# Kernel tuning notes

Hardware: AMD Instinct MI355X
Metric: run time of the kernel (lower is better)

## Reference

```python
import jax, jax.numpy as jnp
import numpy as np

EPS = 1e-5
CONV_THRESHOLD = 0.0


def setup_inputs() -> dict:
    key = jax.random.key(0)
    ks = jax.random.split(key, 16)
    B, F = 65536, 256
    H1, H2 = 1024, 512
    d_in = F + 1  # raw features + 1 scalar conv feature
    inp = {
        "x": jax.random.normal(ks[0], (B, F), dtype=jnp.float32),
        # layer 1: Linear(d_in, H1) + BatchNorm1d(H1)
        "W1": jax.random.normal(ks[1], (d_in, H1), dtype=jnp.float32) * (1.0 / np.sqrt(d_in)),
        "b1": jax.random.normal(ks[2], (H1,), dtype=jnp.float32) * 0.01,
        "g1": jnp.ones((H1,), jnp.float32) + 0.1 * jax.random.normal(ks[3], (H1,), dtype=jnp.float32),
        "be1": jax.random.normal(ks[4], (H1,), dtype=jnp.float32) * 0.01,
        "m1": jax.random.normal(ks[5], (H1,), dtype=jnp.float32) * 0.1,
        "v1": jax.random.uniform(ks[6], (H1,), dtype=jnp.float32, minval=0.5, maxval=1.5),
        # layer 2: Linear(H1, H2) + BatchNorm1d(H2)
        "W2": jax.random.normal(ks[7], (H1, H2), dtype=jnp.float32) * (1.0 / np.sqrt(H1)),
        "b2": jax.random.normal(ks[8], (H2,), dtype=jnp.float32) * 0.01,
        "g2": jnp.ones((H2,), jnp.float32) + 0.1 * jax.random.normal(ks[9], (H2,), dtype=jnp.float32),
        "be2": jax.random.normal(ks[10], (H2,), dtype=jnp.float32) * 0.01,
        "m2": jax.random.normal(ks[11], (H2,), dtype=jnp.float32) * 0.1,
        "v2": jax.random.uniform(ks[12], (H2,), dtype=jnp.float32, minval=0.5, maxval=1.5),
        # output head: Linear(H2, 1)
        "W3": jax.random.normal(ks[13], (H2, 1), dtype=jnp.float32) * (1.0 / np.sqrt(H2)),
        "b3": jax.random.normal(ks[14], (1,), dtype=jnp.float32) * 0.01,
    }
    return inp


def _bn(h, g, be, m, v):
    # eval-mode BatchNorm1d with running statistics
    return g * (h - m) * jax.lax.rsqrt(v + EPS) + be


def reference(x, W1, b1, g1, be1, m1, v1, W2, b2, g2, be2, m2, v2, W3, b3):
    # Batched replacement of the per-sample numpy threshold conv:
    # the Conv filter reduces the whole sample patch with a mean and thresholds it,
    # producing one binary scalar feature per sample.  [B, 1]
    conv_feat = jnp.where(jnp.mean(x, axis=1, keepdims=True) > CONV_THRESHOLD, 1.0, 0.0).astype(x.dtype)
    h = jnp.concatenate([x, conv_feat], axis=1)  # [B, F+1]
    h = jax.nn.relu(_bn(h @ W1 + b1, g1, be1, m1, v1))  # [B, H1]
    h = jax.nn.relu(_bn(h @ W2 + b2, g2, be2, m2, v2))  # [B, H2]
    return jax.nn.sigmoid(h @ W3 + b3)  # [B, 1]
```

## Files before the change

kernel.cpp:

```cpp
#include <hip/hip_runtime.h>
#include <hip/hip_bf16.h>
#include <hip/hip_cooperative_groups.h>
#include <cstdint>
#include <cstddef>

namespace cg = cooperative_groups;

typedef __bf16 bf16_t;
typedef bf16_t bf16x8 __attribute__((ext_vector_type(8)));
typedef float f32x4 __attribute__((ext_vector_type(4)));

#define BN_EPS 1e-5f

__device__ __forceinline__ void async_load16(const bf16_t* g, bf16_t* lds) {
  __builtin_amdgcn_global_load_lds(
      (__attribute__((address_space(1))) uint32_t*)(g),
      (__attribute__((address_space(3))) uint32_t*)(lds),
      16, 0, 0);
}

__global__ void prep_weights_kernel(const float* __restrict__ W1, const float* __restrict__ W2,
                                    const float* b1, const float* g1, const float* be1,
                                    const float* m1, const float* v1,
                                    const float* b2, const float* g2, const float* be2,
                                    const float* m2, const float* v2,
                                    bf16_t* __restrict__ W1T, bf16_t* __restrict__ W2T,
                                    float* s1, float* t1, float* s2, float* t2,
                                    float* w1last) {
  const int b = blockIdx.x;
  if (b < 192) {
    const float* src;
    bf16_t* dst;
    int R, C, bx, by;
    if (b < 64) { src = W1; dst = W1T; R = 256; C = 1024; bx = b & 15; by = b >> 4; }
    else        { src = W2; dst = W2T; R = 1024; C = 512; bx = (b - 64) & 7; by = (b - 64) >> 3; }
    __shared__ bf16_t tile[64][66];
    const int r0 = by * 64, c0 = bx * 64;
    const int tc = threadIdx.x & 63;
    const int tr4 = threadIdx.x >> 6;
#pragma unroll
    for (int i = 0; i < 16; ++i) {
      int r = i * 4 + tr4;
      tile[r][tc] = (bf16_t)src[(size_t)(r0 + r) * C + c0 + tc];
    }
    __syncthreads();
#pragma unroll
    for (int i = 0; i < 16; ++i) {
      int rr = i * 4 + tr4;
      dst[(size_t)(c0 + rr) * R + r0 + tc] = tile[tc][rr];
    }
  } else {
    for (int i = threadIdx.x; i < 1024; i += 256) {
      float s = g1[i] * rsqrtf(v1[i] + BN_EPS);
      s1[i] = s;
      t1[i] = be1[i] - m1[i] * s + b1[i] * s;
      w1last[i] = W1[256 * 1024 + i];
      if (i < 512) {
        float s2v = g2[i] * rsqrtf(v2[i] + BN_EPS);
        s2[i] = s2v;
        t2[i] = be2[i] - m2[i] * s2v + b2[i] * s2v;
      }
    }
  }
}

__device__ __forceinline__ void gemm1_body(
    const float* __restrict__ x, const bf16_t* __restrict__ W1T,
    const float* __restrict__ s1, const float* __restrict__ t1,
    const float* __restrict__ w1last, bf16_t* __restrict__ h1,
    unsigned char* smem, int mTile, int lane, int w) {
  bf16_t* As = (bf16_t*)smem;
  bf16_t* Bs = (bf16_t*)(smem + 65536);
  float* convs = (float*)(smem + 65536);
  const int l15 = lane & 15;
  const int quad = lane >> 4;

  {
    const int rsub = lane >> 5;
    const int c = lane & 31;
#pragma unroll
    for (int i = 0; i < 16; ++i) {
      int row = w * 32 + i * 2 + rsub;
      const float* gx = x + (size_t)(mTile + row) * 256 + c * 8;
      const float4 a = *(const float4*)gx;
      const float4 bq = *(const float4*)(gx + 4);
      float s = a.x + a.y + a.z + a.w + bq.x + bq.y + bq.z + bq.w;
      bf16x8 v = {(bf16_t)a.x, (bf16_t)a.y, (bf16_t)a.z, (bf16_t)a.w,
                  (bf16_t)bq.x, (bf16_t)bq.y, (bf16_t)bq.z, (bf16_t)bq.w};
      *(bf16x8*)(As + row * 256 + (c ^ (row & 7)) * 8) = v;
#pragma unroll
      for (int m = 1; m <= 16; m <<= 1) s += __shfl_xor(s, m);
      if (c == 0) convs[row] = (s > 0.0f) ? 1.0f : 0.0f;
    }
  }
  __syncthreads();

  unsigned cmask = 0;
#pragma unroll
  for (int ti = 0; ti < 8; ++ti)
#pragma unroll
    for (int r = 0; r < 4; ++r)
      if (convs[ti * 16 + quad * 4 + r] > 0.5f) cmask |= (1u << (ti * 4 + r));
  __syncthreads();

  bf16_t* BsW = Bs + w * 2048;
  const int srow = lane >> 2;
  const int schunk = (lane & 3) ^ ((lane >> 3) & 3);
  const int rchunk = quad ^ ((l15 >> 1) & 3);

  for (int j = 0; j < 4; ++j) {
    const int colbase = j * 256 + w * 64;
    f32x4 acc[8][4];
#pragma unroll
    for (int i = 0; i < 8; ++i)
#pragma unroll
      for (int t = 0; t < 4; ++t) {
        f32x4 z = {0.f, 0.f, 0.f, 0.f};
        acc[i][t] = z;
      }

    const bf16_t* gB = W1T + (size_t)(colbase + srow) * 256 + schunk * 8;

#pragma unroll
    for (int i = 0; i < 4; ++i)
      async_load16(gB + (size_t)(i * 16) * 256, BsW + i * 512 + lane * 8);

    for (int ks = 0; ks < 8; ++ks) {
      asm volatile("s_waitcnt vmcnt(0)" ::: "memory");

      bf16x8 af[8], bfr[4];
#pragma unroll
      for (int tj = 0; tj < 4; ++tj)
        bfr[tj] = *(const bf16x8*)(BsW + (tj * 16 + l15) * 32 + rchunk * 8);
#pragma unroll
      for (int ti = 0; ti < 8; ++ti)
        af[ti] = *(const bf16x8*)(As + (ti * 16 + l15) * 256 + ((ks * 4 + quad) ^ (l15 & 7)) * 8);

      asm volatile("s_waitcnt lgkmcnt(0)" ::: "memory");
      if (ks < 7) {
#pragma unroll
        for (int i = 0; i < 4; ++i)
          async_load16(gB + (size_t)(i * 16) * 256 + (ks + 1) * 32, BsW + i * 512 + lane * 8);
      }

      __builtin_amdgcn_s_setprio(1);
#pragma unroll
      for (int ti = 0; ti < 8; ++ti)
#pragma unroll
        for (int tj = 0; tj < 4; ++tj)
          acc[ti][tj] = __builtin_amdgcn_mfma_f32_16x16x32_bf16(af[ti], bfr[tj], acc[ti][tj], 0, 0, 0);
      __builtin_amdgcn_s_setprio(0);
    }

    float sc[4], tcv[4], wl[4];
#pragma unroll
    for (int tj = 0; tj < 4; ++tj) {
      int c = colbase + tj * 16 + l15;
      sc[tj] = s1[c];
      tcv[tj] = t1[c];
      wl[tj] = w1last[c];
    }
#pragma unroll
    for (int ti = 0; ti < 8; ++ti)
#pragma unroll
      for (int r = 0; r < 4; ++r) {
        int row = mTile + ti * 16 + quad * 4 + r;
        size_t base = (size_t)row * 1024 + colbase;
        const float cfv = ((cmask >> (ti * 4 + r)) & 1u) ? 1.0f : 0.0f;
#pragma unroll
        for (int tj = 0; tj < 4; ++tj) {
          float z = acc[ti][tj][r] + cfv * wl[tj];
          z = fmaxf(z * sc[tj] + tcv[tj], 0.f);
          h1[base + tj * 16 + l15] = (bf16_t)z;
        }
      }
  }
}

__device__ __forceinline__ void gemm2_task_body(
    const bf16_t* __restrict__ h1, const bf16_t* __restrict__ W2T,
    const float* __restrict__ s2, const float* __restrict__ t2,
    const float* __restrict__ W3, float* __restrict__ partials,
    unsigned char* smem, int task, int lane, int w) {
  bf16_t* As2 = (bf16_t*)smem;
  bf16_t* Bs2 = (bf16_t*)(smem + 49152);
  const int l15 = lane & 15;
  const int quad = lane >> 4;
  const int sRow = lane >> 2;
  const int sColSwz = ((lane & 3) ^ ((lane >> 3) & 3)) * 8;
  const int rchunk8 = (quad ^ ((l15 >> 1) & 3)) * 8;

  const int mt = (task >> 5) * 8 + (task & 7);
  const int mTile2 = mt * 256;
  const int nt = (task >> 3) & 3;
  const int nTile = nt * 128;

  const bf16_t* gA = h1 + (size_t)(mTile2 + w * 64 + sRow) * 1024 + sColSwz;
  const bf16_t* gB = W2T + (size_t)(nTile + w * 32 + sRow) * 1024 + sColSwz;
  bf16_t* lA0 = As2 + (w * 64) * 32;
  bf16_t* lB0 = Bs2 + (w * 32) * 32;

  f32x4 acc[4][8];
#pragma unroll
  for (int i = 0; i < 4; ++i)
#pragma unroll
    for (int j = 0; j < 8; ++j) {
      f32x4 z = {0.f, 0.f, 0.f, 0.f};
      acc[i][j] = z;
    }

  __syncthreads();

#define STAGE2(aoff, boff, k0)                                              \
  do {                                                                      \
    bf16_t* lA = lA0 + (aoff);                                              \
    bf16_t* lB = lB0 + (boff);                                              \
    async_load16(gA + (k0), lA);                                            \
    async_load16(gA + (size_t)16 * 1024 + (k0), lA + 16 * 32);              \
    async_load16(gA + (size_t)32 * 1024 + (k0), lA + 32 * 32);              \
    async_load16(gA + (size_t)48 * 1024 + (k0), lA + 48 * 32);              \
    async_load16(gB + (k0), lB);                                            \
    async_load16(gB + (size_t)16 * 1024 + (k0), lB + 16 * 32);              \
  } while (0)

  STAGE2(0, 0, 0);
  STAGE2(8192, 4096, 32);

  int aCur = 0, aN1 = 8192, aN2 = 16384;
  int bCur = 0, bN1 = 4096, bN2 = 8192;

  for (int t = 0; t < 32; ++t) {
    if (t < 30) {
      STAGE2(aN2, bN2, (t + 2) * 32);
      asm volatile("s_waitcnt vmcnt(12)" ::: "memory");
    } else if (t == 30) {
      asm volatile("s_waitcnt vmcnt(6)" ::: "memory");
    } else {
      asm volatile("s_waitcnt vmcnt(0)" ::: "memory");
    }
    asm volatile("s_barrier" ::: "memory");

    bf16x8 af[4], bfr[8];
#pragma unroll
    for (int ti = 0; ti < 4; ++ti)
      af[ti] = *(const bf16x8*)(As2 + aCur + (w * 64 + ti * 16 + l15) * 32 + rchunk8);
#pragma unroll
    for (int tj = 0; tj < 8; ++tj)
      bfr[tj] = *(const bf16x8*)(Bs2 + bCur + (tj * 16 + l15) * 32 + rchunk8);

    __builtin_amdgcn_s_setprio(1);
#pragma unroll
    for (int ti = 0; ti < 4; ++ti)
#pragma unroll
      for (int tj = 0; tj < 8; ++tj)
        acc[ti][tj] = __builtin_amdgcn_mfma_f32_16x16x32_bf16(af[ti], bfr[tj], acc[ti][tj], 0, 0, 0);
    __builtin_amdgcn_s_setprio(0);

    asm volatile("s_barrier" ::: "memory");

    int tmp = aCur; aCur = aN1; aN1 = aN2; aN2 = tmp;
    tmp = bCur; bCur = bN1; bN1 = bN2; bN2 = tmp;
  }
#undef STAGE2

  float sc[8], tcs[8], w3c[8];
#pragma unroll
  for (int tj = 0; tj < 8; ++tj) {
    int c = nTile + tj * 16 + l15;
    sc[tj] = s2[c];
    tcs[tj] = t2[c];
    w3c[tj] = W3[c];
  }
#pragma unroll
  for (int ti = 0; ti < 4; ++ti)
#pragma unroll
    for (int r = 0; r < 4; ++r) {
      float pv = 0.f;
#pragma unroll
      for (int tj = 0; tj < 8; ++tj) {
        float z = fmaxf(acc[ti][tj][r] * sc[tj] + tcs[tj], 0.f);
        pv += z * w3c[tj];
      }
#pragma unroll
      for (int m = 1; m <= 8; m <<= 1) pv += __shfl_xor(pv, m);
      if (l15 == 0)
        partials[(size_t)nt * 65536 + mTile2 + w * 64 + ti * 16 + quad * 4 + r] = pv;
    }
}

__global__ __launch_bounds__(256, 2) void gemm1_kernel(
    const float* __restrict__ x, const bf16_t* __restrict__ W1T,
    const float* __restrict__ s1, const float* __restrict__ t1,
    const float* __restrict__ w1last, bf16_t* __restrict__ h1) {
  __shared__ __align__(16) unsigned char smem[81920];
  gemm1_body(x, W1T, s1, t1, w1last, h1, smem, blockIdx.x * 128,
             threadIdx.x & 63, threadIdx.x >> 6);
}

__global__ __launch_bounds__(256, 2) void gemm2_kernel(
    const bf16_t* __restrict__ h1, const bf16_t* __restrict__ W2T,
    const float* __restrict__ s2, const float* __restrict__ t2,
    const float* __restrict__ W3, float* __restrict__ partials) {
  __shared__ __align__(16) unsigned char smem[73728];
  gemm2_task_body(h1, W2T, s2, t2, W3, partials, smem, blockIdx.x,
                  threadIdx.x & 63, threadIdx.x >> 6);
}

__global__ void sigmoid_partials_kernel(const float* __restrict__ partials,
                                        const float* __restrict__ b3,
                                        float* __restrict__ out) {
  int i = blockIdx.x * 256 + threadIdx.x;
  float z = partials[i] + partials[65536 + i] + partials[2 * 65536 + i] +
            partials[3 * 65536 + i] + b3[0];
  out[i] = 1.0f / (1.0f + expf(-z));
}

__global__ __launch_bounds__(256, 2) void fused_mlp_coop(
    const float* __restrict__ x,
    const bf16_t* __restrict__ W1T, const bf16_t* __restrict__ W2T,
    const float* __restrict__ s1, const float* __restrict__ t1,
    const float* __restrict__ w1last,
    const float* __restrict__ s2, const float* __restrict__ t2,
    const float* __restrict__ W3, const float* __restrict__ b3,
    bf16_t* __restrict__ h1, float* __restrict__ partials,
    float* __restrict__ out) {
  __shared__ __align__(16) unsigned char smem[81920];
  cg::grid_group grid = cg::this_grid();
  const int tid = threadIdx.x;
  const int lane = tid & 63;
  const int w = tid >> 6;

  gemm1_body(x, W1T, s1, t1, w1last, h1, smem, blockIdx.x * 128, lane, w);

  grid.sync();

  gemm2_task_body(h1, W2T, s2, t2, W3, partials, smem, blockIdx.x, lane, w);
  gemm2_task_body(h1, W2T, s2, t2, W3, partials, smem, blockIdx.x + 512, lane, w);

  grid.sync();

  if (tid < 128) {
    int r = blockIdx.x * 128 + tid;
    float z = partials[r] + partials[65536 + r] + partials[2 * 65536 + r] +
              partials[3 * 65536 + r] + b3[0];
    out[r] = 1.0f / (1.0f + expf(-z));
  }
}

extern "C" void kernel_launch(void* const* d_in, const int* in_sizes, int n_in,
                              void* d_out, int out_size, void* d_ws, size_t ws_size,
                              hipStream_t stream) {
  const float* x = (const float*)d_in[0];
  const float* W1 = (const float*)d_in[1];
  const float* b1 = (const float*)d_in[2];
  const float* g1 = (const float*)d_in[3];
  const float* be1 = (const float*)d_in[4];
  const float* m1 = (const float*)d_in[5];
  const float* v1 = (const float*)d_in[6];
  const float* W2 = (const float*)d_in[7];
  const float* b2 = (const float*)d_in[8];
  const float* g2 = (const float*)d_in[9];
  const float* be2 = (const float*)d_in[10];
  const float* m2 = (const float*)d_in[11];
  const float* v2 = (const float*)d_in[12];
  const float* W3 = (const float*)d_in[13];
  const float* b3 = (const float*)d_in[14];
  float* out = (float*)d_out;

  char* p = (char*)d_ws;
  bf16_t* h1 = (bf16_t*)p;       p += (size_t)65536 * 1024 * 2;
  float* partials = (float*)p;   p += (size_t)4 * 65536 * 4;
  bf16_t* W1T = (bf16_t*)p;      p += (size_t)1024 * 256 * 2;
  bf16_t* W2T = (bf16_t*)p;      p += (size_t)512 * 1024 * 2;
  float* w1last = (float*)p;     p += 1024 * 4;
  float* s1 = (float*)p;         p += 1024 * 4;
  float* t1 = (float*)p;         p += 1024 * 4;
  float* s2 = (float*)p;         p += 512 * 4;
  float* t2 = (float*)p;         p += 512 * 4;

  prep_weights_kernel<<<193, 256, 0, stream>>>(W1, W2, b1, g1, be1, m1, v1,
                                               b2, g2, be2, m2, v2,
                                               W1T, W2T, s1, t1, s2, t2, w1last);

  int dev = 0;
  (void)hipGetDevice(&dev);
  int coopOk = 0;
  (void)hipDeviceGetAttribute(&coopOk, hipDeviceAttributeCooperativeLaunch, dev);
  int numCU = 0;
  (void)hipDeviceGetAttribute(&numCU, hipDeviceAttributeMultiprocessorCount, dev);
  int maxBlk = 0;
  (void)hipOccupancyMaxActiveBlocksPerMultiprocessor(&maxBlk, fused_mlp_coop, 256, 0);

  bool useCoop = (coopOk != 0) && ((long)maxBlk * (long)numCU >= 512L);
  if (useCoop) {
    void* args[] = {(void*)&x, (void*)&W1T, (void*)&W2T, (void*)&s1, (void*)&t1,
                    (void*)&w1last, (void*)&s2, (void*)&t2, (void*)&W3, (void*)&b3,
                    (void*)&h1, (void*)&partials, (void*)&out};
    hipError_t e = hipLaunchCooperativeKernel((const void*)fused_mlp_coop,
                                              dim3(512), dim3(256), args, 0, stream);
    if (e != hipSuccess) useCoop = false;
  }
  if (!useCoop) {
    gemm1_kernel<<<512, 256, 0, stream>>>(x, W1T, s1, t1, w1last, h1);
    gemm2_kernel<<<1024, 256, 0, stream>>>(h1, W2T, s2, t2, W3, partials);
    sigmoid_partials_kernel<<<256, 256, 0, stream>>>(partials, b3, out);
  }
}
```

Measured before the change: 262.6 us.

## Fuse both GEMMs per 64-row tile, drop cooperative grid syncs

Replaces the cooperative kernel and its two grid-wide syncs with a normal 1024-block kernel. Each block computes its own 64-row slice of h1, then immediately runs the second GEMM on those rows, which are likely still in L2. The output head and sigmoid run in-block, so the global partials buffer goes away. Smaller tiles allow three blocks per CU, but each block now reloads all of W2T and the second GEMM uses a 64x256 tile with double buffering, which lowers reuse of the weights.

Measured after the change: 261.5 us. Within noise of the previous version (-0.4%).

```diff
diff --git a/kernel.cpp b/kernel.cpp
--- a/kernel.cpp
+++ b/kernel.cpp
@@ -1,10 +1,7 @@
 #include <hip/hip_runtime.h>
 #include <hip/hip_bf16.h>
-#include <hip/hip_cooperative_groups.h>
 #include <cstdint>
 #include <cstddef>
-
-namespace cg = cooperative_groups;
 
 typedef __bf16 bf16_t;
 typedef bf16_t bf16x8 __attribute__((ext_vector_type(8)));
@@ -64,23 +61,32 @@
   }
 }
 
-__device__ __forceinline__ void gemm1_body(
-    const float* __restrict__ x, const bf16_t* __restrict__ W1T,
+__global__ __launch_bounds__(256, 3) void fused_mlp(
+    const float* __restrict__ x,
+    const bf16_t* __restrict__ W1T, const bf16_t* __restrict__ W2T,
     const float* __restrict__ s1, const float* __restrict__ t1,
-    const float* __restrict__ w1last, bf16_t* __restrict__ h1,
-    unsigned char* smem, int mTile, int lane, int w) {
-  bf16_t* As = (bf16_t*)smem;
-  bf16_t* Bs = (bf16_t*)(smem + 65536);
-  float* convs = (float*)(smem + 65536);
+    const float* __restrict__ w1last,
+    const float* __restrict__ s2, const float* __restrict__ t2,
+    const float* __restrict__ W3, const float* __restrict__ b3,
+    bf16_t* __restrict__ h1, float* __restrict__ out) {
+  __shared__ __align__(16) unsigned char smem[49152];
+  const int tid = threadIdx.x;
+  const int lane = tid & 63;
+  const int w = tid >> 6;
   const int l15 = lane & 15;
   const int quad = lane >> 4;
+  const int mTile = blockIdx.x * 64;
+
+  bf16_t* As = (bf16_t*)smem;
+  bf16_t* Bs = (bf16_t*)(smem + 32768);
+  float* convs = (float*)(smem + 32768);
 
   {
     const int rsub = lane >> 5;
     const int c = lane & 31;
 #pragma unroll
-    for (int i = 0; i < 16; ++i) {
-      int row = w * 32 + i * 2 + rsub;
+    for (int i = 0; i < 8; ++i) {
+      int row = w * 16 + i * 2 + rsub;
       const float* gx = x + (size_t)(mTile + row) * 256 + c * 8;
       const float4 a = *(const float4*)gx;
       const float4 bq = *(const float4*)(gx + 4);
@@ -97,7 +103,7 @@
 
   unsigned cmask = 0;
 #pragma unroll
-  for (int ti = 0; ti < 8; ++ti)
+  for (int ti = 0; ti < 4; ++ti)
 #pragma unroll
     for (int r = 0; r < 4; ++r)
       if (convs[ti * 16 + quad * 4 + r] > 0.5f) cmask |= (1u << (ti * 4 + r));
@@ -110,9 +116,9 @@
 
   for (int j = 0; j < 4; ++j) {
     const int colbase = j * 256 + w * 64;
-    f32x4 acc[8][4];
-#pragma unroll
-    for (int i = 0; i < 8; ++i)
+    f32x4 acc[4][4];
+#pragma unroll
+    for (int i = 0; i < 4; ++i)
 #pragma unroll
       for (int t = 0; t < 4; ++t) {
         f32x4 z = {0.f, 0.f, 0.f, 0.f};
@@ -128,12 +134,12 @@
     for (int ks = 0; ks < 8; ++ks) {
       asm volatile("s_waitcnt vmcnt(0)" ::: "memory");
 
-      bf16x8 af[8], bfr[4];
+      bf16x8 af[4], bfr[4];
 #pragma unroll
       for (int tj = 0; tj < 4; ++tj)
         bfr[tj] = *(const bf16x8*)(BsW + (tj * 16 + l15) * 32 + rchunk * 8);
 #pragma unroll
-      for (int ti = 0; ti < 8; ++ti)
+      for (int ti = 0; ti < 4; ++ti)
         af[ti] = *(const bf16x8*)(As + (ti * 16 + l15) * 256 + ((ks * 4 + quad) ^ (l15 & 7)) * 8);
 
       asm volatile("s_waitcnt lgkmcnt(0)" ::: "memory");
@@ -145,7 +151,7 @@
 
       __builtin_amdgcn_s_setprio(1);
 #pragma unroll
-      for (int ti = 0; ti < 8; ++ti)
+      for (int ti = 0; ti < 4; ++ti)
 #pragma unroll
         for (int tj = 0; tj < 4; ++tj)
           acc[ti][tj] = __builtin_amdgcn_mfma_f32_16x16x32_bf16(af[ti], bfr[tj], acc[ti][tj], 0, 0, 0);
@@ -161,7 +167,7 @@
       wl[tj] = w1last[c];
     }
 #pragma unroll
-    for (int ti = 0; ti < 8; ++ti)
+    for (int ti = 0; ti < 4; ++ti)
 #pragma unroll
       for (int r = 0; r < 4; ++r) {
         int row = mTile + ti * 16 + quad * 4 + r;
@@ -175,175 +181,115 @@
         }
       }
   }
-}
-
-__device__ __forceinline__ void gemm2_task_body(
-    const bf16_t* __restrict__ h1, const bf16_t* __restrict__ W2T,
-    const float* __restrict__ s2, const float* __restrict__ t2,
-    const float* __restrict__ W3, float* __restrict__ partials,
-    unsigned char* smem, int task, int lane, int w) {
-  bf16_t* As2 = (bf16_t*)smem;
-  bf16_t* Bs2 = (bf16_t*)(smem + 49152);
-  const int l15 = lane & 15;
-  const int quad = lane >> 4;
-  const int sRow = lane >> 2;
-  const int sColSwz = ((lane & 3) ^ ((lane >> 3) & 3)) * 8;
-  const int rchunk8 = (quad ^ ((l15 >> 1) & 3)) * 8;
-
-  const int mt = (task >> 5) * 8 + (task & 7);
-  const int mTile2 = mt * 256;
-  const int nt = (task >> 3) & 3;
-  const int nTile = nt * 128;
-
-  const bf16_t* gA = h1 + (size_t)(mTile2 + w * 64 + sRow) * 1024 + sColSwz;
-  const bf16_t* gB = W2T + (size_t)(nTile + w * 32 + sRow) * 1024 + sColSwz;
-  bf16_t* lA0 = As2 + (w * 64) * 32;
-  bf16_t* lB0 = Bs2 + (w * 32) * 32;
-
-  f32x4 acc[4][8];
-#pragma unroll
-  for (int i = 0; i < 4; ++i)
-#pragma unroll
-    for (int j = 0; j < 8; ++j) {
-      f32x4 z = {0.f, 0.f, 0.f, 0.f};
-      acc[i][j] = z;
-    }
-
+
+  asm volatile("s_waitcnt vmcnt(0)" ::: "memory");
+
+  bf16_t* A2 = (bf16_t*)smem;
+  bf16_t* B2 = (bf16_t*)(smem + 8192);
+  float* outW = (float*)(smem + 40960);
+  const int rchunk8 = rchunk * 8;
+  const int sColSwz = schunk * 8;
+
+  float rowpv[4][4];
+#pragma unroll
+  for (int ti = 0; ti < 4; ++ti)
+#pragma unroll
+    for (int r = 0; r < 4; ++r) rowpv[ti][r] = 0.f;
+
+  for (int nt = 0; nt < 2; ++nt) {
+    __syncthreads();
+
+    const bf16_t* gA = h1 + (size_t)(mTile + w * 16 + srow) * 1024 + sColSwz;
+    const bf16_t* gB2 = W2T + (size_t)(nt * 256 + w * 64 + srow) * 1024 + sColSwz;
+
+    f32x4 acc2[4][4];
+#pragma unroll
+    for (int i = 0; i < 4; ++i)
+#pragma unroll
+      for (int t = 0; t < 4; ++t) {
+        f32x4 z = {0.f, 0.f, 0.f, 0.f};
+        acc2[i][t] = z;
+      }
+
+#define STAGE2(buf, k0)                                                       \
+  do {                                                                        \
+    async_load16(gA + (k0), A2 + (buf)*2048 + w * 512 + lane * 8);            \
+    async_load16(gB2 + (k0), B2 + (buf)*8192 + w * 2048 + lane * 8);          \
+    async_load16(gB2 + (size_t)16 * 1024 + (k0),                              \
+                 B2 + (buf)*8192 + w * 2048 + 512 + lane * 8);                \
+    async_load16(gB2 + (size_t)32 * 1024 + (k0),                              \
+                 B2 + (buf)*8192 + w * 2048 + 1024 + lane * 8);               \
+    async_load16(gB2 + (size_t)48 * 1024 + (k0),                              \
+                 B2 + (buf)*8192 + w * 2048 + 1536 + lane * 8);               \
+  } while (0)
+
+    STAGE2(0, 0);
+    int buf = 0;
+    for (int t = 0; t < 32; ++t) {
+      if (t < 31) {
+        STAGE2(buf ^ 1, (t + 1) * 32);
+        asm volatile("s_waitcnt vmcnt(5)" ::: "memory");
+      } else {
+        asm volatile("s_waitcnt vmcnt(0)" ::: "memory");
+      }
+      asm volatile("s_barrier" ::: "memory");
+
+      bf16x8 af[4], bfr[4];
+#pragma unroll
+      for (int ti = 0; ti < 4; ++ti)
+        af[ti] = *(const bf16x8*)(A2 + buf * 2048 + (ti * 16 + l15) * 32 + rchunk8);
+#pragma unroll
+      for (int tj = 0; tj < 4; ++tj)
+        bfr[tj] = *(const bf16x8*)(B2 + buf * 8192 + (w * 64 + tj * 16 + l15) * 32 + rchunk8);
+
+      __builtin_amdgcn_s_setprio(1);
+#pragma unroll
+      for (int ti = 0; ti < 4; ++ti)
+#pragma unroll
+        for (int tj = 0; tj < 4; ++tj)
+          acc2[ti][tj] = __builtin_amdgcn_mfma_f32_16x16x32_bf16(af[ti], bfr[tj], acc2[ti][tj], 0, 0, 0);
+      __builtin_amdgcn_s_setprio(0);
+
+      asm volatile("s_barrier" ::: "memory");
+      buf ^= 1;
+    }
+#undef STAGE2
+
+    float sc[4], tcs[4], w3c[4];
+#pragma unroll
+    for (int tj = 0; tj < 4; ++tj) {
+      int c = nt * 256 + w * 64 + tj * 16 + l15;
+      sc[tj] = s2[c];
+      tcs[tj] = t2[c];
+      w3c[tj] = W3[c];
+    }
+#pragma unroll
+    for (int ti = 0; ti < 4; ++ti)
+#pragma unroll
+      for (int r = 0; r < 4; ++r) {
+        float pv = 0.f;
+#pragma unroll
+        for (int tj = 0; tj < 4; ++tj) {
+          float z = fmaxf(acc2[ti][tj][r] * sc[tj] + tcs[tj], 0.f);
+          pv += z * w3c[tj];
+        }
+#pragma unroll
+        for (int m = 1; m <= 8; m <<= 1) pv += __shfl_xor(pv, m);
+        rowpv[ti][r] += pv;
+      }
+  }
+
+  if (l15 == 0) {
+#pragma unroll
+    for (int ti = 0; ti < 4; ++ti)
+#pragma unroll
+      for (int r = 0; r < 4; ++r)
+        outW[w * 64 + ti * 16 + quad * 4 + r] = rowpv[ti][r];
+  }
   __syncthreads();
-
-#define STAGE2(aoff, boff, k0)                                              \
-  do {                                                                      \
-    bf16_t* lA = lA0 + (aoff);                                              \
-    bf16_t* lB = lB0 + (boff);                                              \
-    async_load16(gA + (k0), lA);                                            \
-    async_load16(gA + (size_t)16 * 1024 + (k0), lA + 16 * 32);              \
-    async_load16(gA + (size_t)32 * 1024 + (k0), lA + 32 * 32);              \
-    async_load16(gA + (size_t)48 * 1024 + (k0), lA + 48 * 32);              \
-    async_load16(gB + (k0), lB);                                            \
-    async_load16(gB + (size_t)16 * 1024 + (k0), lB + 16 * 32);              \
-  } while (0)
-
-  STAGE2(0, 0, 0);
-  STAGE2(8192, 4096, 32);
-
-  int aCur = 0, aN1 = 8192, aN2 = 16384;
-  int bCur = 0, bN1 = 4096, bN2 = 8192;
-
-  for (int t = 0; t < 32; ++t) {
-    if (t < 30) {
-      STAGE2(aN2, bN2, (t + 2) * 32);
-      asm volatile("s_waitcnt vmcnt(12)" ::: "memory");
-    } else if (t == 30) {
-      asm volatile("s_waitcnt vmcnt(6)" ::: "memory");
-    } else {
-      asm volatile("s_waitcnt vmcnt(0)" ::: "memory");
-    }
-    asm volatile("s_barrier" ::: "memory");
-
-    bf16x8 af[4], bfr[8];
-#pragma unroll
-    for (int ti = 0; ti < 4; ++ti)
-      af[ti] = *(const bf16x8*)(As2 + aCur + (w * 64 + ti * 16 + l15) * 32 + rchunk8);
-#pragma unroll
-    for (int tj = 0; tj < 8; ++tj)
-      bfr[tj] = *(const bf16x8*)(Bs2 + bCur + (tj * 16 + l15) * 32 + rchunk8);
-
-    __builtin_amdgcn_s_setprio(1);
-#pragma unroll
-    for (int ti = 0; ti < 4; ++ti)
-#pragma unroll
-      for (int tj = 0; tj < 8; ++tj)
-        acc[ti][tj] = __builtin_amdgcn_mfma_f32_16x16x32_bf16(af[ti], bfr[tj], acc[ti][tj], 0, 0, 0);
-    __builtin_amdgcn_s_setprio(0);
-
-    asm volatile("s_barrier" ::: "memory");
-
-    int tmp = aCur; aCur = aN1; aN1 = aN2; aN2 = tmp;
-    tmp = bCur; bCur = bN1; bN1 = bN2; bN2 = tmp;
-  }
-#undef STAGE2
-
-  float sc[8], tcs[8], w3c[8];
-#pragma unroll
-  for (int tj = 0; tj < 8; ++tj) {
-    int c = nTile + tj * 16 + l15;
-    sc[tj] = s2[c];
-    tcs[tj] = t2[c];
-    w3c[tj] = W3[c];
-  }
-#pragma unroll
-  for (int ti = 0; ti < 4; ++ti)
-#pragma unroll
-    for (int r = 0; r < 4; ++r) {
-      float pv = 0.f;
-#pragma unroll
-      for (int tj = 0; tj < 8; ++tj) {
-        float z = fmaxf(acc[ti][tj][r] * sc[tj] + tcs[tj], 0.f);
-        pv += z * w3c[tj];
-      }
-#pragma unroll
-      for (int m = 1; m <= 8; m <<= 1) pv += __shfl_xor(pv, m);
-      if (l15 == 0)
-        partials[(size_t)nt * 65536 + mTile2 + w * 64 + ti * 16 + quad * 4 + r] = pv;
-    }
-}
-
-__global__ __launch_bounds__(256, 2) void gemm1_kernel(
-    const float* __restrict__ x, const bf16_t* __restrict__ W1T,
-    const float* __restrict__ s1, const float* __restrict__ t1,
-    const float* __restrict__ w1last, bf16_t* __restrict__ h1) {
-  __shared__ __align__(16) unsigned char smem[81920];
-  gemm1_body(x, W1T, s1, t1, w1last, h1, smem, blockIdx.x * 128,
-             threadIdx.x & 63, threadIdx.x >> 6);
-}
-
-__global__ __launch_bounds__(256, 2) void gemm2_kernel(
-    const bf16_t* __restrict__ h1, const bf16_t* __restrict__ W2T,
-    const float* __restrict__ s2, const float* __restrict__ t2,
-    const float* __restrict__ W3, float* __restrict__ partials) {
-  __shared__ __align__(16) unsigned char smem[73728];
-  gemm2_task_body(h1, W2T, s2, t2, W3, partials, smem, blockIdx.x,
-                  threadIdx.x & 63, threadIdx.x >> 6);
-}
-
-__global__ void sigmoid_partials_kernel(const float* __restrict__ partials,
-                                        const float* __restrict__ b3,
-                                        float* __restrict__ out) {
-  int i = blockIdx.x * 256 + threadIdx.x;
-  float z = partials[i] + partials[65536 + i] + partials[2 * 65536 + i] +
-            partials[3 * 65536 + i] + b3[0];
-  out[i] = 1.0f / (1.0f + expf(-z));
-}
-
-__global__ __launch_bounds__(256, 2) void fused_mlp_coop(
-    const float* __restrict__ x,
-    const bf16_t* __restrict__ W1T, const bf16_t* __restrict__ W2T,
-    const float* __restrict__ s1, const float* __restrict__ t1,
-    const float* __restrict__ w1last,
-    const float* __restrict__ s2, const float* __restrict__ t2,
-    const float* __restrict__ W3, const float* __restrict__ b3,
-    bf16_t* __restrict__ h1, float* __restrict__ partials,
-    float* __restrict__ out) {
-  __shared__ __align__(16) unsigned char smem[81920];
-  cg::grid_group grid = cg::this_grid();
-  const int tid = threadIdx.x;
-  const int lane = tid & 63;
-  const int w = tid >> 6;
-
-  gemm1_body(x, W1T, s1, t1, w1last, h1, smem, blockIdx.x * 128, lane, w);
-
-  grid.sync();
-
-  gemm2_task_body(h1, W2T, s2, t2, W3, partials, smem, blockIdx.x, lane, w);
-  gemm2_task_body(h1, W2T, s2, t2, W3, partials, smem, blockIdx.x + 512, lane, w);
-
-  grid.sync();
-
-  if (tid < 128) {
-    int r = blockIdx.x * 128 + tid;
-    float z = partials[r] + partials[65536 + r] + partials[2 * 65536 + r] +
-              partials[3 * 65536 + r] + b3[0];
-    out[r] = 1.0f / (1.0f + expf(-z));
+  if (tid < 64) {
+    float z = outW[tid] + outW[64 + tid] + outW[128 + tid] + outW[192 + tid] + b3[0];
+    out[mTile + tid] = 1.0f / (1.0f + expf(-z));
   }
 }
 
@@ -377,32 +323,12 @@
   float* t1 = (float*)p;         p += 1024 * 4;
   float* s2 = (float*)p;         p += 512 * 4;
   float* t2 = (float*)p;         p += 512 * 4;
+  (void)partials;
 
   prep_weights_kernel<<<193, 256, 0, stream>>>(W1, W2, b1, g1, be1, m1, v1,
                                                b2, g2, be2, m2, v2,
                                                W1T, W2T, s1, t1, s2, t2, w1last);
 
-  int dev = 0;
-  (void)hipGetDevice(&dev);
-  int coopOk = 0;
-  (void)hipDeviceGetAttribute(&coopOk, hipDeviceAttributeCooperativeLaunch, dev);
-  int numCU = 0;
-  (void)hipDeviceGetAttribute(&numCU, hipDeviceAttributeMultiprocessorCount, dev);
-  int maxBlk = 0;
-  (void)hipOccupancyMaxActiveBlocksPerMultiprocessor(&maxBlk, fused_mlp_coop, 256, 0);
-
-  bool useCoop = (coopOk != 0) && ((long)maxBlk * (long)numCU >= 512L);
-  if (useCoop) {
-    void* args[] = {(void*)&x, (void*)&W1T, (void*)&W2T, (void*)&s1, (void*)&t1,
-                    (void*)&w1last, (void*)&s2, (void*)&t2, (void*)&W3, (void*)&b3,
-                    (void*)&h1, (void*)&partials, (void*)&out};
-    hipError_t e = hipLaunchCooperativeKernel((const void*)fused_mlp_coop,
-                                              dim3(512), dim3(256), args, 0, stream);
-    if (e != hipSuccess) useCoop = false;
-  }
-  if (!useCoop) {
-    gemm1_kernel<<<512, 256, 0, stream>>>(x, W1T, s1, t1, w1last, h1);
-    gemm2_kernel<<<1024, 256, 0, stream>>>(h1, W2T, s2, t2, W3, partials);
-    sigmoid_partials_kernel<<<256, 256, 0, stream>>>(partials, b3, out);
-  }
+  fused_mlp<<<1024, 256, 0, stream>>>(x, W1T, W2T, s1, t1, w1last,
+                                      s2, t2, W3, b3, h1, out);
 }
```
